# Kernel tuning notes

Measured on AMD Instinct MI355X. Metric: run time of the kernel, lower is better.

## Reference

```python
import jax, jax.numpy as jnp
import numpy as np

B, N, E, F, H, K, C, G = 64, 2048, 16384, 32, 64, 8, 16, 64


def setup_inputs() -> dict:
    key = jax.random.key(0)
    ks = jax.random.split(key, 10)
    s = lambda fan: 1.0 / np.sqrt(fan)
    return {
        "x": jax.random.normal(ks[0], (B, N, C), jnp.float32),
        "linc": (jax.random.uniform(ks[1], (N, E)) < (8.0 / N)).astype(jnp.float32),
        "rinc": (jax.random.uniform(ks[2], (E, N)) < (8.0 / N)).astype(jnp.float32),
        "ef": jax.random.normal(ks[3], (E, F), jnp.float32),
        "w1": jax.random.uniform(ks[4], (H, F), jnp.float32, -s(F), s(F)),
        "b1": jax.random.uniform(ks[5], (H,), jnp.float32, -s(F), s(F)),
        "w2": jax.random.uniform(ks[6], (K, H), jnp.float32, -s(H), s(H)),
        "b2": jax.random.uniform(ks[7], (K,), jnp.float32, -s(H), s(H)),
        "gcw": jax.random.uniform(ks[8], (G, C * K), jnp.float32, -s(C * K), s(C * K)),
        "gcb": jax.random.uniform(ks[9], (G,), jnp.float32, -s(C * K), s(C * K)),
    }


def reference(x, linc, rinc, ef, w1, b1, w2, b2, gcw, gcb):
    # edge MLP -> per-edge kernel weights [E, K]
    h = jax.nn.relu(ef @ w1.T + b1)
    w = h @ w2.T + b2
    # structurally: y_k = linc @ diag(w[:,k]) @ rinc @ x, without building [K,N,N]
    z = jnp.einsum('en,bnc->bec', rinc, x)                  # gather: node -> edge
    y = jnp.einsum('ne,ek,bec->bnck', linc, w, z)           # scale + scatter: edge -> node
    b = x.shape[0]
    y = y.reshape(b, N, C * K)                              # matches permute(0,2,-1,1).reshape
    out = jax.nn.relu(y @ gcw.T + gcb)                      # [B, N, G]
    return out.reshape(b, -1)
```

## Files before the change

### kernel.cpp

```cpp
#include <hip/hip_runtime.h>
#include <hip/hip_bf16.h>

#define B_ 64
#define N_ 2048
#define E_ 16384
#define F_ 32
#define H_ 64
#define K_ 8
#define C_ 16
#define G_ 64
#define CK 128
#define CAP 120
#define RCAP 32
#define YLD 136
#define BC 1024

typedef __attribute__((ext_vector_type(8))) short bf16x8;
typedef __attribute__((ext_vector_type(8))) unsigned short u16x8;
typedef __attribute__((ext_vector_type(4))) float f32x4;

__device__ inline float bf2f(unsigned short u) {
  union { unsigned int i; float f; } v; v.i = ((unsigned int)u) << 16; return v.f;
}
__device__ inline unsigned short f2bf(float f) {
  union { float f; unsigned int i; } v; v.f = f;
  unsigned int x = v.i;
  return (unsigned short)((x + 0x7fffu + ((x >> 16) & 1u)) >> 16);
}

__global__ __launch_bounds__(256) void xpose_k(
    const float* __restrict__ x, const float* __restrict__ gcw,
    unsigned short* __restrict__ x_t, unsigned short* __restrict__ gcw_bf,
    int* __restrict__ cnts ) {
  int t = threadIdx.x;
  int blk = blockIdx.x;
  if (blk >= N_) {
    if (blk == N_) {
      for (int i = t; i < G_*CK; i += 256) gcw_bf[i] = f2bf(gcw[i]);
    } else {
      int zid = blk - (N_ + 1);
      for (int i = zid*256 + t; i < N_ + E_; i += 8*256) cnts[i] = 0;
    }
    return;
  }
  int n = blk;
  int b = t >> 2, c0 = (t & 3) * 4;
  float4 xv = *(const float4*)(x + (size_t)b*(N_*C_) + (size_t)n*C_ + c0);
  ushort4 o;
  o.x = f2bf(xv.x); o.y = f2bf(xv.y); o.z = f2bf(xv.z); o.w = f2bf(xv.w);
  *(ushort4*)&x_t[(size_t)n*BC + 4*t] = o;
}

__global__ __launch_bounds__(256) void scan_k(
    const float* __restrict__ linc, const float* __restrict__ rinc,
    int* __restrict__ lcnt, unsigned short* __restrict__ lidx,
    int* __restrict__ rcnt, unsigned short* __restrict__ ridx) {
  int t = threadIdx.x;
  int blk = blockIdx.x;
  if (blk < N_) {
    int n = blk;
    const f32x4* row = (const f32x4*)(linc + (size_t)n*E_);
    unsigned short* lrow = lidx + (size_t)n*CAP;
    #pragma unroll
    for (int j = 0; j < E_/4/256; j++) {
      int i = t + 256*j;
      f32x4 v = __builtin_nontemporal_load(row + i);
      if (v.x != 0.f) { int p = atomicAdd(&lcnt[n],1); if (p<CAP) lrow[p] = (unsigned short)(i*4+0); }
      if (v.y != 0.f) { int p = atomicAdd(&lcnt[n],1); if (p<CAP) lrow[p] = (unsigned short)(i*4+1); }
      if (v.z != 0.f) { int p = atomicAdd(&lcnt[n],1); if (p<CAP) lrow[p] = (unsigned short)(i*4+2); }
      if (v.w != 0.f) { int p = atomicAdd(&lcnt[n],1); if (p<CAP) lrow[p] = (unsigned short)(i*4+3); }
    }
  } else {
    int e0 = (blk - N_) * 8;
    const f32x4* base = (const f32x4*)(rinc + (size_t)e0*N_);
    #pragma unroll
    for (int j = 0; j < 8*N_/4/256; j++) {
      int i = t + 256*j;
      f32x4 v = __builtin_nontemporal_load(base + i);
      int e = e0 + (i >> 9);
      int nn = (i & 511) * 4;
      unsigned short* rrow = ridx + (size_t)e*RCAP;
      if (v.x != 0.f) { int p = atomicAdd(&rcnt[e],1); if (p<RCAP) rrow[p] = (unsigned short)(nn+0); }
      if (v.y != 0.f) { int p = atomicAdd(&rcnt[e],1); if (p<RCAP) rrow[p] = (unsigned short)(nn+1); }
      if (v.z != 0.f) { int p = atomicAdd(&rcnt[e],1); if (p<RCAP) rrow[p] = (unsigned short)(nn+2); }
      if (v.w != 0.f) { int p = atomicAdd(&rcnt[e],1); if (p<RCAP) rrow[p] = (unsigned short)(nn+3); }
    }
  }
}

__global__ __launch_bounds__(256) void edge_mlp_k(
    const float* __restrict__ ef, const float* __restrict__ w1,
    const float* __restrict__ b1, const float* __restrict__ w2,
    const float* __restrict__ b2, float* __restrict__ w_out) {
  __shared__ float s_w1[H_*F_];
  __shared__ float s_w2[K_*H_];
  __shared__ float s_b1[H_];
  __shared__ float s_b2[K_];
  int t = threadIdx.x;
  for (int i = t; i < H_*F_; i += 256) s_w1[i] = w1[i];
  for (int i = t; i < K_*H_; i += 256) s_w2[i] = w2[i];
  if (t < H_) s_b1[t] = b1[t];
  if (t < K_) s_b2[t] = b2[t];
  __syncthreads();
  int e = blockIdx.x*256 + t;
  float efr[F_];
  const float4* efp = (const float4*)(ef + (size_t)e*F_);
  #pragma unroll
  for (int f4 = 0; f4 < F_/4; f4++) {
    float4 v = efp[f4];
    efr[f4*4+0]=v.x; efr[f4*4+1]=v.y; efr[f4*4+2]=v.z; efr[f4*4+3]=v.w;
  }
  float acc[K_];
  #pragma unroll
  for (int k = 0; k < K_; k++) acc[k] = s_b2[k];
  #pragma unroll 4
  for (int h = 0; h < H_; h++) {
    float hv = s_b1[h];
    #pragma unroll
    for (int f = 0; f < F_; f++) hv = fmaf(efr[f], s_w1[h*F_+f], hv);
    hv = fmaxf(hv, 0.f);
    #pragma unroll
    for (int k = 0; k < K_; k++) acc[k] = fmaf(hv, s_w2[k*H_+h], acc[k]);
  }
  #pragma unroll
  for (int k = 0; k < K_; k++) w_out[(size_t)e*K_ + k] = acc[k];
}

__global__ __launch_bounds__(256) void gather_z_k(
    const int* __restrict__ rcnt, const unsigned short* __restrict__ ridx,
    const unsigned short* __restrict__ x_t, unsigned short* __restrict__ z) {
  int t = threadIdx.x, wv = t >> 6, lane = t & 63;
  int e = blockIdx.x * 4 + wv;
  int cnt = min(rcnt[e], RCAP);
  int my = 0;
  if (lane < cnt) my = ridx[(size_t)e*RCAP + lane];
  const unsigned short* xb = x_t + 16*lane;
  float acc[16];
  #pragma unroll
  for (int k = 0; k < 16; k++) acc[k] = 0.f;
  for (int i = 0; i < cnt; i++) {
    int n = __shfl(my, i);
    u16x8 a0 = *(const u16x8*)(xb + (size_t)n*BC);
    u16x8 a1 = *(const u16x8*)(xb + (size_t)n*BC + 8);
    #pragma unroll
    for (int k = 0; k < 8; k++) { acc[k] += bf2f(a0[k]); acc[8+k] += bf2f(a1[k]); }
  }
  u16x8 o0, o1;
  #pragma unroll
  for (int k = 0; k < 8; k++) { o0[k] = f2bf(acc[k]); o1[k] = f2bf(acc[8+k]); }
  unsigned short* zp = z + (size_t)e*BC + 16*lane;
  *(u16x8*)zp = o0;
  *(u16x8*)(zp + 8) = o1;
}

__global__ __launch_bounds__(256, 6) void node_out_k(
    const int* __restrict__ lcnt, const unsigned short* __restrict__ lidx,
    const unsigned short* __restrict__ z, const float* __restrict__ w,
    const unsigned short* __restrict__ gcw_bf, const float* __restrict__ gcb,
    float* __restrict__ out) {
  __shared__ unsigned short s_y[B_*YLD];
  __shared__ float s_w[CAP*K_];
  __shared__ float s_gcb[G_];
  __shared__ int   s_idx[CAP];
  int t = threadIdx.x;
  int n = blockIdx.x;
  if (t < G_) s_gcb[t] = gcb[t];

  int cnt = min(lcnt[n], CAP);
  const unsigned short* lrow = lidx + (size_t)n*CAP;
  for (int i = t; i < cnt; i += 256) s_idx[i] = lrow[i];
  for (int i = t; i < cnt*K_; i += 256)
    s_w[i] = w[(size_t)lrow[i >> 3]*K_ + (i & 7)];
  __syncthreads();

  float acc[4][K_];
  #pragma unroll
  for (int j = 0; j < 4; j++)
    #pragma unroll
    for (int k = 0; k < K_; k++) acc[j][k] = 0.f;
  const unsigned short* zt = z + 4*t;
  for (int i = 0; i < cnt; i++) {
    int e = s_idx[i];
    const float4* wp = (const float4*)&s_w[i*K_];
    float4 w0 = wp[0], w1v = wp[1];
    float we[K_] = {w0.x, w0.y, w0.z, w0.w, w1v.x, w1v.y, w1v.z, w1v.w};
    ushort4 zu = *(const ushort4*)(zt + (size_t)e*BC);
    float zv[4] = {bf2f(zu.x), bf2f(zu.y), bf2f(zu.z), bf2f(zu.w)};
    #pragma unroll
    for (int j = 0; j < 4; j++)
      #pragma unroll
      for (int k = 0; k < K_; k++) acc[j][k] = fmaf(zv[j], we[k], acc[j][k]);
  }
  {
    int b = t >> 2, ckb = (t & 3) * 32;
    #pragma unroll
    for (int j = 0; j < 4; j++) {
      ushort4 lo, hi;
      lo.x = f2bf(acc[j][0]); lo.y = f2bf(acc[j][1]); lo.z = f2bf(acc[j][2]); lo.w = f2bf(acc[j][3]);
      hi.x = f2bf(acc[j][4]); hi.y = f2bf(acc[j][5]); hi.z = f2bf(acc[j][6]); hi.w = f2bf(acc[j][7]);
      *(ushort4*)&s_y[b*YLD + ckb + 8*j]     = lo;
      *(ushort4*)&s_y[b*YLD + ckb + 8*j + 4] = hi;
    }
  }
  __syncthreads();

  {
    int wv = t >> 6, lane = t & 63;
    int m = lane & 15, q = lane >> 4;
    f32x4 cf0 = {0.f,0.f,0.f,0.f}, cf1 = cf0, cf2 = cf0, cf3 = cf0;
    #pragma unroll
    for (int ks = 0; ks < 4; ks++) {
      bf16x8 a = *(const bf16x8*)&s_y[(16*wv + m)*YLD + 32*ks + 8*q];
      bf16x8 b0 = *(const bf16x8*)&gcw_bf[(size_t)(m     )*CK + 32*ks + 8*q];
      bf16x8 b1 = *(const bf16x8*)&gcw_bf[(size_t)(16 + m)*CK + 32*ks + 8*q];
      bf16x8 b2 = *(const bf16x8*)&gcw_bf[(size_t)(32 + m)*CK + 32*ks + 8*q];
      bf16x8 b3 = *(const bf16x8*)&gcw_bf[(size_t)(48 + m)*CK + 32*ks + 8*q];
      cf0 = __builtin_amdgcn_mfma_f32_16x16x32_bf16(a, b0, cf0, 0, 0, 0);
      cf1 = __builtin_amdgcn_mfma_f32_16x16x32_bf16(a, b1, cf1, 0, 0, 0);
      cf2 = __builtin_amdgcn_mfma_f32_16x16x32_bf16(a, b2, cf2, 0, 0, 0);
      cf3 = __builtin_amdgcn_mfma_f32_16x16x32_bf16(a, b3, cf3, 0, 0, 0);
    }
    float* ob = out + (size_t)n*G_;
    #pragma unroll
    for (int r = 0; r < 4; r++) {
      int b = 16*wv + 4*q + r;
      float* op = ob + (size_t)b*(N_*G_);
      float v0 = fmaxf(cf0[r] + s_gcb[m],      0.f);
      float v1 = fmaxf(cf1[r] + s_gcb[16 + m], 0.f);
      float v2 = fmaxf(cf2[r] + s_gcb[32 + m], 0.f);
      float v3 = fmaxf(cf3[r] + s_gcb[48 + m], 0.f);
      op[m]      = v0;
      op[16 + m] = v1;
      op[32 + m] = v2;
      op[48 + m] = v3;
    }
  }
}

extern "C" void kernel_launch(void* const* d_in, const int* in_sizes, int n_in,
                              void* d_out, int out_size, void* d_ws, size_t ws_size,
                              hipStream_t stream) {
  const float* x    = (const float*)d_in[0];
  const float* linc = (const float*)d_in[1];
  const float* rinc = (const float*)d_in[2];
  const float* ef   = (const float*)d_in[3];
  const float* w1   = (const float*)d_in[4];
  const float* b1   = (const float*)d_in[5];
  const float* w2   = (const float*)d_in[6];
  const float* b2   = (const float*)d_in[7];
  const float* gcw  = (const float*)d_in[8];
  const float* gcb  = (const float*)d_in[9];
  float* out = (float*)d_out;

  char* ws = (char*)d_ws;
  float* w_e             = (float*)ws;            ws += (size_t)E_*K_*sizeof(float);
  unsigned short* z      = (unsigned short*)ws;   ws += (size_t)E_*BC*sizeof(short);
  unsigned short* x_t    = (unsigned short*)ws;   ws += (size_t)N_*BC*sizeof(short);
  unsigned short* gcw_bf = (unsigned short*)ws;   ws += (size_t)G_*CK*sizeof(short);
  int* lcnt              = (int*)ws;              ws += (size_t)N_*sizeof(int);
  int* rcnt              = (int*)ws;              ws += (size_t)E_*sizeof(int);
  unsigned short* lidx   = (unsigned short*)ws;   ws += (size_t)N_*CAP*sizeof(short);
  unsigned short* ridx   = (unsigned short*)ws;   ws += (size_t)E_*RCAP*sizeof(short);

  xpose_k<<<N_ + 1 + 8, 256, 0, stream>>>(x, gcw, x_t, gcw_bf, lcnt);
  scan_k<<<N_ + E_/8, 256, 0, stream>>>(linc, rinc, lcnt, lidx, rcnt, ridx);
  edge_mlp_k<<<E_/256, 256, 0, stream>>>(ef, w1, b1, w2, b2, w_e);
  gather_z_k<<<E_/4, 256, 0, stream>>>(rcnt, ridx, x_t, z);
  node_out_k<<<N_, 256, 0, stream>>>(lcnt, lidx, z, w_e, gcw_bf, gcb, out);
}
```

Measured before the change: 393.5 us.

## Fuse prep kernels, build sparse lists in LDS, fuse rinc scan with gather

Merges the x transpose, gcw conversion, edge MLP and linc row scan into a single prep kernel. Row index lists are now built with LDS atomics instead of global atomics, so the counter-zeroing pass and the global rcnt/ridx buffers go away. The rinc scan is fused into the gather kernel, so each block scans 8 edges and immediately gathers x_t for them, which removes two kernel launches and a global round trip. The cost is that the gather now waits behind the scan inside each block, giving less latency hiding between the two phases.

```diff
diff --git a/kernel.cpp b/kernel.cpp
--- a/kernel.cpp
+++ b/kernel.cpp
@@ -28,129 +28,133 @@
   return (unsigned short)((x + 0x7fffu + ((x >> 16) & 1u)) >> 16);
 }
 
-__global__ __launch_bounds__(256) void xpose_k(
+__global__ __launch_bounds__(256) void prep_k(
     const float* __restrict__ x, const float* __restrict__ gcw,
+    const float* __restrict__ ef, const float* __restrict__ w1,
+    const float* __restrict__ b1, const float* __restrict__ w2,
+    const float* __restrict__ b2, const float* __restrict__ linc,
     unsigned short* __restrict__ x_t, unsigned short* __restrict__ gcw_bf,
-    int* __restrict__ cnts ) {
+    float* __restrict__ w_out, int* __restrict__ lcnt,
+    unsigned short* __restrict__ lidx) {
   int t = threadIdx.x;
   int blk = blockIdx.x;
-  if (blk >= N_) {
-    if (blk == N_) {
-      for (int i = t; i < G_*CK; i += 256) gcw_bf[i] = f2bf(gcw[i]);
-    } else {
-      int zid = blk - (N_ + 1);
-      for (int i = zid*256 + t; i < N_ + E_; i += 8*256) cnts[i] = 0;
-    }
-    return;
-  }
-  int n = blk;
-  int b = t >> 2, c0 = (t & 3) * 4;
-  float4 xv = *(const float4*)(x + (size_t)b*(N_*C_) + (size_t)n*C_ + c0);
-  ushort4 o;
-  o.x = f2bf(xv.x); o.y = f2bf(xv.y); o.z = f2bf(xv.z); o.w = f2bf(xv.w);
-  *(ushort4*)&x_t[(size_t)n*BC + 4*t] = o;
-}
-
-__global__ __launch_bounds__(256) void scan_k(
-    const float* __restrict__ linc, const float* __restrict__ rinc,
-    int* __restrict__ lcnt, unsigned short* __restrict__ lidx,
-    int* __restrict__ rcnt, unsigned short* __restrict__ ridx) {
-  int t = threadIdx.x;
-  int blk = blockIdx.x;
+
   if (blk < N_) {
     int n = blk;
+    int b = t >> 2, c0 = (t & 3) * 4;
+    float4 xv = *(const float4*)(x + (size_t)b*(N_*C_) + (size_t)n*C_ + c0);
+    ushort4 o;
+    o.x = f2bf(xv.x); o.y = f2bf(xv.y); o.z = f2bf(xv.z); o.w = f2bf(xv.w);
+    *(ushort4*)&x_t[(size_t)n*BC + 4*t] = o;
+    return;
+  }
+  if (blk == N_) {
+    for (int i = t; i < G_*CK; i += 256) gcw_bf[i] = f2bf(gcw[i]);
+    return;
+  }
+  if (blk <= N_ + E_/256) {
+    __shared__ float s_w1[H_*F_];
+    __shared__ float s_w2[K_*H_];
+    __shared__ float s_b1[H_];
+    __shared__ float s_b2[K_];
+    for (int i = t; i < H_*F_; i += 256) s_w1[i] = w1[i];
+    for (int i = t; i < K_*H_; i += 256) s_w2[i] = w2[i];
+    if (t < H_) s_b1[t] = b1[t];
+    if (t < K_) s_b2[t] = b2[t];
+    __syncthreads();
+    int e = (blk - N_ - 1)*256 + t;
+    float efr[F_];
+    const float4* efp = (const float4*)(ef + (size_t)e*F_);
+    #pragma unroll
+    for (int f4 = 0; f4 < F_/4; f4++) {
+      float4 v = efp[f4];
+      efr[f4*4+0]=v.x; efr[f4*4+1]=v.y; efr[f4*4+2]=v.z; efr[f4*4+3]=v.w;
+    }
+    float acc[K_];
+    #pragma unroll
+    for (int k = 0; k < K_; k++) acc[k] = s_b2[k];
+    #pragma unroll 4
+    for (int h = 0; h < H_; h++) {
+      float hv = s_b1[h];
+      #pragma unroll
+      for (int f = 0; f < F_; f++) hv = fmaf(efr[f], s_w1[h*F_+f], hv);
+      hv = fmaxf(hv, 0.f);
+      #pragma unroll
+      for (int k = 0; k < K_; k++) acc[k] = fmaf(hv, s_w2[k*H_+h], acc[k]);
+    }
+    #pragma unroll
+    for (int k = 0; k < K_; k++) w_out[(size_t)e*K_ + k] = acc[k];
+    return;
+  }
+  {
+    __shared__ unsigned short s_list[CAP];
+    __shared__ int s_cnt;
+    int n = blk - (N_ + E_/256 + 1);
+    if (t == 0) s_cnt = 0;
+    __syncthreads();
     const f32x4* row = (const f32x4*)(linc + (size_t)n*E_);
-    unsigned short* lrow = lidx + (size_t)n*CAP;
     #pragma unroll
     for (int j = 0; j < E_/4/256; j++) {
       int i = t + 256*j;
       f32x4 v = __builtin_nontemporal_load(row + i);
-      if (v.x != 0.f) { int p = atomicAdd(&lcnt[n],1); if (p<CAP) lrow[p] = (unsigned short)(i*4+0); }
-      if (v.y != 0.f) { int p = atomicAdd(&lcnt[n],1); if (p<CAP) lrow[p] = (unsigned short)(i*4+1); }
-      if (v.z != 0.f) { int p = atomicAdd(&lcnt[n],1); if (p<CAP) lrow[p] = (unsigned short)(i*4+2); }
-      if (v.w != 0.f) { int p = atomicAdd(&lcnt[n],1); if (p<CAP) lrow[p] = (unsigned short)(i*4+3); }
-    }
-  } else {
-    int e0 = (blk - N_) * 8;
-    const f32x4* base = (const f32x4*)(rinc + (size_t)e0*N_);
-    #pragma unroll
-    for (int j = 0; j < 8*N_/4/256; j++) {
-      int i = t + 256*j;
-      f32x4 v = __builtin_nontemporal_load(base + i);
-      int e = e0 + (i >> 9);
-      int nn = (i & 511) * 4;
-      unsigned short* rrow = ridx + (size_t)e*RCAP;
-      if (v.x != 0.f) { int p = atomicAdd(&rcnt[e],1); if (p<RCAP) rrow[p] = (unsigned short)(nn+0); }
-      if (v.y != 0.f) { int p = atomicAdd(&rcnt[e],1); if (p<RCAP) rrow[p] = (unsigned short)(nn+1); }
-      if (v.z != 0.f) { int p = atomicAdd(&rcnt[e],1); if (p<RCAP) rrow[p] = (unsigned short)(nn+2); }
-      if (v.w != 0.f) { int p = atomicAdd(&rcnt[e],1); if (p<RCAP) rrow[p] = (unsigned short)(nn+3); }
-    }
-  }
-}
-
-__global__ __launch_bounds__(256) void edge_mlp_k(
-    const float* __restrict__ ef, const float* __restrict__ w1,
-    const float* __restrict__ b1, const float* __restrict__ w2,
-    const float* __restrict__ b2, float* __restrict__ w_out) {
-  __shared__ float s_w1[H_*F_];
-  __shared__ float s_w2[K_*H_];
-  __shared__ float s_b1[H_];
-  __shared__ float s_b2[K_];
+      if (v.x != 0.f) { int p = atomicAdd(&s_cnt,1); if (p<CAP) s_list[p] = (unsigned short)(i*4+0); }
+      if (v.y != 0.f) { int p = atomicAdd(&s_cnt,1); if (p<CAP) s_list[p] = (unsigned short)(i*4+1); }
+      if (v.z != 0.f) { int p = atomicAdd(&s_cnt,1); if (p<CAP) s_list[p] = (unsigned short)(i*4+2); }
+      if (v.w != 0.f) { int p = atomicAdd(&s_cnt,1); if (p<CAP) s_list[p] = (unsigned short)(i*4+3); }
+    }
+    __syncthreads();
+    int cnt = min(s_cnt, CAP);
+    if (t == 0) lcnt[n] = cnt;
+    for (int i = t; i < cnt; i += 256) lidx[(size_t)n*CAP + i] = s_list[i];
+  }
+}
+
+__global__ __launch_bounds__(256) void scan_gather_k(
+    const float* __restrict__ rinc, const unsigned short* __restrict__ x_t,
+    unsigned short* __restrict__ z) {
+  __shared__ unsigned short s_list[8][RCAP];
+  __shared__ int s_cnt[8];
   int t = threadIdx.x;
-  for (int i = t; i < H_*F_; i += 256) s_w1[i] = w1[i];
-  for (int i = t; i < K_*H_; i += 256) s_w2[i] = w2[i];
-  if (t < H_) s_b1[t] = b1[t];
-  if (t < K_) s_b2[t] = b2[t];
-  __syncthreads();
-  int e = blockIdx.x*256 + t;
-  float efr[F_];
-  const float4* efp = (const float4*)(ef + (size_t)e*F_);
+  int e0 = blockIdx.x * 8;
+  if (t < 8) s_cnt[t] = 0;
+  __syncthreads();
+  const f32x4* base = (const f32x4*)(rinc + (size_t)e0*N_);
   #pragma unroll
-  for (int f4 = 0; f4 < F_/4; f4++) {
-    float4 v = efp[f4];
-    efr[f4*4+0]=v.x; efr[f4*4+1]=v.y; efr[f4*4+2]=v.z; efr[f4*4+3]=v.w;
-  }
-  float acc[K_];
+  for (int j = 0; j < 8*N_/4/256; j++) {
+    int i = t + 256*j;
+    f32x4 v = __builtin_nontemporal_load(base + i);
+    int er = i >> 9;
+    int nn = (i & 511) * 4;
+    if (v.x != 0.f) { int p = atomicAdd(&s_cnt[er],1); if (p<RCAP) s_list[er][p] = (unsigned short)(nn+0); }
+    if (v.y != 0.f) { int p = atomicAdd(&s_cnt[er],1); if (p<RCAP) s_list[er][p] = (unsigned short)(nn+1); }
+    if (v.z != 0.f) { int p = atomicAdd(&s_cnt[er],1); if (p<RCAP) s_list[er][p] = (unsigned short)(nn+2); }
+    if (v.w != 0.f) { int p = atomicAdd(&s_cnt[er],1); if (p<RCAP) s_list[er][p] = (unsigned short)(nn+3); }
+  }
+  __syncthreads();
+  int wv = t >> 6, lane = t & 63;
+  const unsigned short* xb = x_t + 16*lane;
   #pragma unroll
-  for (int k = 0; k < K_; k++) acc[k] = s_b2[k];
-  #pragma unroll 4
-  for (int h = 0; h < H_; h++) {
-    float hv = s_b1[h];
-    #pragma unroll
-    for (int f = 0; f < F_; f++) hv = fmaf(efr[f], s_w1[h*F_+f], hv);
-    hv = fmaxf(hv, 0.f);
-    #pragma unroll
-    for (int k = 0; k < K_; k++) acc[k] = fmaf(hv, s_w2[k*H_+h], acc[k]);
-  }
-  #pragma unroll
-  for (int k = 0; k < K_; k++) w_out[(size_t)e*K_ + k] = acc[k];
-}
-
-__global__ __launch_bounds__(256) void gather_z_k(
-    const int* __restrict__ rcnt, const unsigned short* __restrict__ ridx,
-    const unsigned short* __restrict__ x_t, unsigned short* __restrict__ z) {
-  int t = threadIdx.x, wv = t >> 6, lane = t & 63;
-  int e = blockIdx.x * 4 + wv;
-  int cnt = min(rcnt[e], RCAP);
-  int my = 0;
-  if (lane < cnt) my = ridx[(size_t)e*RCAP + lane];
-  const unsigned short* xb = x_t + 16*lane;
-  float acc[16];
-  #pragma unroll
-  for (int k = 0; k < 16; k++) acc[k] = 0.f;
-  for (int i = 0; i < cnt; i++) {
-    int n = __shfl(my, i);
-    u16x8 a0 = *(const u16x8*)(xb + (size_t)n*BC);
-    u16x8 a1 = *(const u16x8*)(xb + (size_t)n*BC + 8);
-    #pragma unroll
-    for (int k = 0; k < 8; k++) { acc[k] += bf2f(a0[k]); acc[8+k] += bf2f(a1[k]); }
-  }
-  u16x8 o0, o1;
-  #pragma unroll
-  for (int k = 0; k < 8; k++) { o0[k] = f2bf(acc[k]); o1[k] = f2bf(acc[8+k]); }
-  unsigned short* zp = z + (size_t)e*BC + 16*lane;
-  *(u16x8*)zp = o0;
-  *(u16x8*)(zp + 8) = o1;
+  for (int rep = 0; rep < 2; rep++) {
+    int er = wv + 4*rep;
+    int e = e0 + er;
+    int cnt = min(s_cnt[er], RCAP);
+    float acc[16];
+    #pragma unroll
+    for (int k = 0; k < 16; k++) acc[k] = 0.f;
+    for (int i = 0; i < cnt; i++) {
+      int n = s_list[er][i];
+      u16x8 a0 = *(const u16x8*)(xb + (size_t)n*BC);
+      u16x8 a1 = *(const u16x8*)(xb + (size_t)n*BC + 8);
+      #pragma unroll
+      for (int k = 0; k < 8; k++) { acc[k] += bf2f(a0[k]); acc[8+k] += bf2f(a1[k]); }
+    }
+    u16x8 o0, o1;
+    #pragma unroll
+    for (int k = 0; k < 8; k++) { o0[k] = f2bf(acc[k]); o1[k] = f2bf(acc[8+k]); }
+    unsigned short* zp = z + (size_t)e*BC + 16*lane;
+    *(u16x8*)zp = o0;
+    *(u16x8*)(zp + 8) = o1;
+  }
 }
 
 __global__ __launch_bounds__(256, 6) void node_out_k(
@@ -169,8 +173,9 @@
   int cnt = min(lcnt[n], CAP);
   const unsigned short* lrow = lidx + (size_t)n*CAP;
   for (int i = t; i < cnt; i += 256) s_idx[i] = lrow[i];
+  __syncthreads();
   for (int i = t; i < cnt*K_; i += 256)
-    s_w[i] = w[(size_t)lrow[i >> 3]*K_ + (i & 7)];
+    s_w[i] = w[(size_t)s_idx[i >> 3]*K_ + (i & 7)];
   __syncthreads();
 
   float acc[4][K_];
@@ -258,13 +263,10 @@
   unsigned short* x_t    = (unsigned short*)ws;   ws += (size_t)N_*BC*sizeof(short);
   unsigned short* gcw_bf = (unsigned short*)ws;   ws += (size_t)G_*CK*sizeof(short);
   int* lcnt              = (int*)ws;              ws += (size_t)N_*sizeof(int);
-  int* rcnt              = (int*)ws;              ws += (size_t)E_*sizeof(int);
   unsigned short* lidx   = (unsigned short*)ws;   ws += (size_t)N_*CAP*sizeof(short);
-  unsigned short* ridx   = (unsigned short*)ws;   ws += (size_t)E_*RCAP*sizeof(short);
-
-  xpose_k<<<N_ + 1 + 8, 256, 0, stream>>>(x, gcw, x_t, gcw_bf, lcnt);
-  scan_k<<<N_ + E_/8, 256, 0, stream>>>(linc, rinc, lcnt, lidx, rcnt, ridx);
-  edge_mlp_k<<<E_/256, 256, 0, stream>>>(ef, w1, b1, w2, b2, w_e);
-  gather_z_k<<<E_/4, 256, 0, stream>>>(rcnt, ridx, x_t, z);
+
+  prep_k<<<N_ + 1 + E_/256 + N_, 256, 0, stream>>>(
+      x, gcw, ef, w1, b1, w2, b2, linc, x_t, gcw_bf, w_e, lcnt, lidx);
+  scan_gather_k<<<E_/8, 256, 0, stream>>>(rinc, x_t, z);
   node_out_k<<<N_, 256, 0, stream>>>(lcnt, lidx, z, w_e, gcw_bf, gcb, out);
 }
```

Result: faster. 370.4 us (-5.9%).
